# Optimization experiments

Hardware: AMD Instinct MI355X
Metric: run time of the kernel (lower is better)

The kernel has to match this reference:

```python
import jax, jax.numpy as jnp
import numpy as np

DIM = 1024
NUM_HEADS = 16
HEAD_DIM = DIM // NUM_HEADS
B, L = 4, 4096


def setup_inputs() -> dict:
    key = jax.random.key(0)
    ks = jax.random.split(key, 11)
    s = 1.0 / np.sqrt(DIM)
    inp = {
        'q_seq': jax.random.normal(ks[0], (B, L, DIM), jnp.float32),
        'k_seq': jax.random.normal(ks[1], (B, L, DIM), jnp.float32),
        'v_seq': jax.random.normal(ks[2], (B, L, DIM), jnp.float32),
        'Wq': jax.random.normal(ks[3], (DIM, DIM), jnp.float32) * s,
        'bq': jax.random.normal(ks[4], (DIM,), jnp.float32) * s,
        'Wk': jax.random.normal(ks[5], (DIM, DIM), jnp.float32) * s,
        'bk': jax.random.normal(ks[6], (DIM,), jnp.float32) * s,
        'Wv': jax.random.normal(ks[7], (DIM, DIM), jnp.float32) * s,
        'bv': jax.random.normal(ks[8], (DIM,), jnp.float32) * s,
        'Wo': jax.random.normal(ks[9], (DIM, DIM), jnp.float32) * s,
        'bo': jax.random.normal(ks[10], (DIM,), jnp.float32) * s,
        'extract_common': 1,
    }
    return inp


def _heads(x):
    # [B, L, DIM] -> [B, H, L, D]
    Bb, Ll, _ = x.shape
    return x.reshape(Bb, Ll, NUM_HEADS, HEAD_DIM).transpose(0, 2, 1, 3)


def reference(q_seq, k_seq, v_seq, Wq, bq, Wk, bk, Wv, bv, Wo, bo, extract_common):
    Q = _heads(q_seq @ Wq.T + bq)   # [B, H, Lq, D]
    K = _heads(k_seq @ Wk.T + bk)   # [B, H, Lk, D]
    V = _heads(v_seq @ Wv.T + bv)   # [B, H, Lv, D]
    # softmax over the sequence dimension of K (torch dim=2 of [B,H,L,D])
    K_probs = jax.nn.softmax(K, axis=2)
    # context = K_probs^T @ V : [B, H, D, D]
    context = jnp.einsum('bhld,bhle->bhde', K_probs, V)
    attended = jnp.einsum('bhld,bhde->bhle', Q, context)  # [B, H, Lq, D]
    if extract_common:
        target = attended
    else:
        target = V - attended
    Bb, _, Ll, _ = target.shape
    target = target.transpose(0, 2, 1, 3).reshape(Bb, Ll, DIM)
    return target @ Wo.T + bo
```

## Files before the change

kernel.cpp:

```cpp
#include <hip/hip_runtime.h>
#include <cmath>

typedef __bf16 bf16x8 __attribute__((ext_vector_type(8)));
typedef float f32x4 __attribute__((ext_vector_type(4)));
typedef unsigned short us8 __attribute__((ext_vector_type(8)));

__device__ __forceinline__ unsigned short f2bf(float f) {
    union { float f; unsigned u; } x; x.f = f;
    unsigned u = x.u + 0x7FFFu + ((x.u >> 16) & 1u);
    return (unsigned short)(u >> 16);
}
__device__ __forceinline__ float bf2f(unsigned short h) {
    union { unsigned u; float f; } x; x.u = ((unsigned)h) << 16;
    return x.f;
}

__device__ __forceinline__ us8 pack8(f32x4 a, f32x4 b) {
    union { bf16x8 h; us8 u; } cv;
    cv.h[0] = (__bf16)a[0]; cv.h[1] = (__bf16)a[1];
    cv.h[2] = (__bf16)a[2]; cv.h[3] = (__bf16)a[3];
    cv.h[4] = (__bf16)b[0]; cv.h[5] = (__bf16)b[1];
    cv.h[6] = (__bf16)b[2]; cv.h[7] = (__bf16)b[3];
    return cv.u;
}

__device__ __forceinline__ us8 cvt8(const float* p) {
    f32x4 a = *(const f32x4*)p;
    f32x4 b = *(const f32x4*)(p + 4);
    return pack8(a, b);
}

__device__ __forceinline__ void gl2lds16(const unsigned short* g, unsigned short* l) {
    __builtin_amdgcn_global_load_lds(
        (const __attribute__((address_space(1))) unsigned int*)g,
        (__attribute__((address_space(3))) unsigned int*)l, 16, 0, 0);
}

__global__ __launch_bounds__(256)
void cvt_kernel(const float* __restrict__ src, unsigned short* __restrict__ dst) {
    const size_t i = ((size_t)blockIdx.x * 256 + threadIdx.x) * 8;
    *(us8*)(dst + i) = cvt8(src + i);
}

__global__ __launch_bounds__(256)
void cvt_w4(const float* __restrict__ s0, const float* __restrict__ s1,
            const float* __restrict__ s2, const float* __restrict__ s3,
            unsigned short* __restrict__ d0, unsigned short* __restrict__ d1,
            unsigned short* __restrict__ d2, unsigned short* __restrict__ d3) {
    const float* sp[4] = {s0, s1, s2, s3};
    unsigned short* dp[4] = {d0, d1, d2, d3};
    const float* src = sp[blockIdx.y];
    unsigned short* dst = dp[blockIdx.y];
    const size_t i = ((size_t)blockIdx.x * 256 + threadIdx.x) * 8;
    *(us8*)(dst + i) = cvt8(src + i);
}

__device__ __forceinline__ void swz_tiles(int& m0, int& n0) {
    const int slot = blockIdx.x + (blockIdx.y << 3);
    const int w = ((slot & 7) << 7) | (slot >> 3);
    m0 = (w >> 3) << 7;
    n0 = (w & 7) << 7;
}

template<int MODE, bool BF>
__global__ __launch_bounds__(256)
void gemm_proj(const void* __restrict__ Ap, const void* __restrict__ Wp,
               const float* __restrict__ bias,
               unsigned short* __restrict__ outT,
               float* __restrict__ S)
{
    __shared__ __align__(16) unsigned short lds[24576];

    const int tid = threadIdx.x;
    const int wid = tid >> 6, lane = tid & 63;
    const int quad = lane >> 4, l16 = lane & 15;
    const int waveM = wid >> 1, waveN = wid & 1;
    int m0, n0; swz_tiles(m0, n0);
    const int srow = tid >> 2, scol = (tid & 3) * 8;
    const int r4 = lane >> 2, c8 = (lane & 3) * 8;

    f32x4 acc[4][4] = {};

    if (BF) {
        const unsigned short* A = (const unsigned short*)Ap;
        const unsigned short* W = (const unsigned short*)Wp;
#define STAGE_P(K0, BASE)                                                     \
        for (int s = wid; s < 8; s += 4) {                                    \
            const int row = s * 16 + r4;                                      \
            gl2lds16(A + (size_t)(m0 + row) * 1024 + (K0) + c8, (BASE) + s * 512);          \
            gl2lds16(W + (size_t)(n0 + row) * 1024 + (K0) + c8, (BASE) + 4096 + s * 512);   \
        }
        STAGE_P(0, lds);
        STAGE_P(32, lds + 8192);
        asm volatile("s_waitcnt vmcnt(4) lgkmcnt(0)" ::: "memory");
        __builtin_amdgcn_s_barrier();

        int cur = 0;
        for (int it = 0; it < 32; ++it) {
            if (it < 30) {
                const int st = (cur >= 1) ? cur - 1 : 2;
                STAGE_P((it + 2) * 32, lds + st * 8192);
            }
            const unsigned short* ldsA = lds + cur * 8192;
            const unsigned short* ldsB = ldsA + 4096;
            bf16x8 af[4], bfr[4];
#pragma unroll
            for (int i = 0; i < 4; ++i)
                af[i] = *(const bf16x8*)(ldsA + (waveM * 64 + i * 16 + l16) * 32 + quad * 8);
#pragma unroll
            for (int j = 0; j < 4; ++j)
                bfr[j] = *(const bf16x8*)(ldsB + (waveN * 64 + j * 16 + l16) * 32 + quad * 8);
#pragma unroll
            for (int i = 0; i < 4; ++i)
#pragma unroll
                for (int j = 0; j < 4; ++j)
                    acc[i][j] = __builtin_amdgcn_mfma_f32_16x16x32_bf16(af[i], bfr[j], acc[i][j], 0, 0, 0);
            if (it < 30) {
                asm volatile("s_waitcnt vmcnt(4) lgkmcnt(0)" ::: "memory");
                __builtin_amdgcn_s_barrier();
            } else if (it == 30) {
                asm volatile("s_waitcnt vmcnt(0) lgkmcnt(0)" ::: "memory");
                __builtin_amdgcn_s_barrier();
            }
            cur = (cur < 2) ? cur + 1 : 0;
        }
#undef STAGE_P
    } else {
        const float* A = (const float*)Ap;
        const float* W = (const float*)Wp;
#pragma unroll
        for (int p = 0; p < 2; ++p) {
            *(us8*)(lds + (p * 64 + srow) * 32 + scol) = cvt8(A + (size_t)(m0 + p * 64 + srow) * 1024 + scol);
            *(us8*)(lds + 4096 + (p * 64 + srow) * 32 + scol) = cvt8(W + (size_t)(n0 + p * 64 + srow) * 1024 + scol);
        }
        __syncthreads();
        int cur = 0;
        for (int k0 = 0; k0 < 1024; k0 += 32) {
            const int nxt = cur ^ 1;
            if (k0 < 992) {
#pragma unroll
                for (int p = 0; p < 2; ++p) {
                    *(us8*)(lds + nxt * 8192 + (p * 64 + srow) * 32 + scol) =
                        cvt8(A + (size_t)(m0 + p * 64 + srow) * 1024 + k0 + 32 + scol);
                    *(us8*)(lds + nxt * 8192 + 4096 + (p * 64 + srow) * 32 + scol) =
                        cvt8(W + (size_t)(n0 + p * 64 + srow) * 1024 + k0 + 32 + scol);
                }
            }
            const unsigned short* ldsA = lds + cur * 8192;
            const unsigned short* ldsB = ldsA + 4096;
            bf16x8 af[4], bfr[4];
#pragma unroll
            for (int i = 0; i < 4; ++i)
                af[i] = *(const bf16x8*)(ldsA + (waveM * 64 + i * 16 + l16) * 32 + quad * 8);
#pragma unroll
            for (int j = 0; j < 4; ++j)
                bfr[j] = *(const bf16x8*)(ldsB + (waveN * 64 + j * 16 + l16) * 32 + quad * 8);
#pragma unroll
            for (int i = 0; i < 4; ++i)
#pragma unroll
                for (int j = 0; j < 4; ++j)
                    acc[i][j] = __builtin_amdgcn_mfma_f32_16x16x32_bf16(af[i], bfr[j], acc[i][j], 0, 0, 0);
            __syncthreads();
            cur = nxt;
        }
    }
    __syncthreads();

    const int b = m0 >> 12, l0 = m0 & 4095;
#pragma unroll
    for (int j = 0; j < 4; ++j) {
        const int nn = waveN * 64 + j * 16 + l16;
        const float bc = bias[n0 + nn];
        float ssum = 0.f;
#pragma unroll
        for (int i = 0; i < 4; ++i)
#pragma unroll
            for (int r = 0; r < 4; ++r) {
                const int mm = waveM * 64 + i * 16 + quad * 4 + r;
                float v = acc[i][j][r] + bc;
                if (MODE == 1) v = expf(fminf(fmaxf(v, -30.f), 30.f));
                lds[nn * 136 + mm] = f2bf(v);
                ssum += v;
            }
        if (MODE == 1) {
            ssum += __shfl_xor(ssum, 16);
            ssum += __shfl_xor(ssum, 32);
            if (lane < 16)
                atomicAdd(&S[(size_t)b * 1024 + n0 + waveN * 64 + j * 16 + lane], ssum);
        }
    }
    __syncthreads();
    const int seg = (tid & 15) * 8;
#pragma unroll
    for (int it = 0; it < 8; ++it) {
        const int nn = (tid >> 4) + it * 16;
        us8 v = *(const us8*)&lds[nn * 136 + seg];
        *(us8*)(outT + ((size_t)b * 1024 + n0 + nn) * 4096 + l0 + seg) = v;
    }
}

__global__ __launch_bounds__(256)
void ctx_kernel(const unsigned short* __restrict__ Vt,
                const unsigned short* __restrict__ Et,
                float* __restrict__ ctxf)
{
    __shared__ __align__(16) unsigned short lds[8192];

    const int tid = threadIdx.x;
    const int wid = tid >> 6, lane = tid & 63;
    const int quad = lane >> 4, l16 = lane & 15;
    const int b = blockIdx.z, h = blockIdx.y;
    const int lbase = blockIdx.x * 512;

    const unsigned short* Arow = Vt + ((size_t)b * 1024 + h * 64) * 4096;
    const unsigned short* Brow = Et + ((size_t)b * 1024 + h * 64) * 4096;

    const int srow = tid >> 2;
    const int scol = (tid & 3) * 8;

    f32x4 acc[4] = {};

    {
        us8 va = *(const us8*)(Arow + (size_t)srow * 4096 + lbase + scol);
        us8 vb = *(const us8*)(Brow + (size_t)srow * 4096 + lbase + scol);
        *(us8*)(lds + srow * 32 + scol) = va;
        *(us8*)(lds + 2048 + srow * 32 + scol) = vb;
    }
    __syncthreads();

    int cur = 0;
    for (int k0 = 0; k0 < 512; k0 += 32) {
        const int nxt = cur ^ 1;
        us8 na = {}, nb = {};
        const bool pf = (k0 < 480);
        if (pf) {
            na = *(const us8*)(Arow + (size_t)srow * 4096 + lbase + k0 + 32 + scol);
            nb = *(const us8*)(Brow + (size_t)srow * 4096 + lbase + k0 + 32 + scol);
        }
        const unsigned short* ldsA = lds + cur * 4096;
        const unsigned short* ldsB = ldsA + 2048;
        bf16x8 a = *(const bf16x8*)(ldsA + (wid * 16 + l16) * 32 + quad * 8);
#pragma unroll
        for (int j = 0; j < 4; ++j) {
            bf16x8 bb = *(const bf16x8*)(ldsB + (j * 16 + l16) * 32 + quad * 8);
            acc[j] = __builtin_amdgcn_mfma_f32_16x16x32_bf16(a, bb, acc[j], 0, 0, 0);
        }
        if (pf) {
            *(us8*)(lds + nxt * 4096 + srow * 32 + scol) = na;
            *(us8*)(lds + nxt * 4096 + 2048 + srow * 32 + scol) = nb;
        }
        __syncthreads();
        cur = nxt;
    }
    float* base = ctxf + ((size_t)(b * 16 + h)) * 4096;
#pragma unroll
    for (int j = 0; j < 4; ++j)
#pragma unroll
        for (int r = 0; r < 4; ++r) {
            const int e = wid * 16 + quad * 4 + r;
            const int d = j * 16 + l16;
            atomicAdd(base + e * 64 + d, acc[j][r]);
        }
}

template<bool BF>
__global__ __launch_bounds__(256)
void gemm_qattn(const void* __restrict__ Ap, const void* __restrict__ Wp,
                const float* __restrict__ bias,
                const float* __restrict__ ctxf,
                const float* __restrict__ Sv,
                const unsigned short* __restrict__ Vt,
                const int* __restrict__ ec,
                unsigned short* __restrict__ att)
{
    __shared__ __align__(16) unsigned short lds[26624];
    unsigned short* ldsQ = lds;
    unsigned short* ldsC = lds + 17408;

    const int tid = threadIdx.x;
    const int wid = tid >> 6, lane = tid & 63;
    const int quad = lane >> 4, l16 = lane & 15;
    const int waveM = wid >> 1, waveN = wid & 1;
    int m0, n0; swz_tiles(m0, n0);
    const int b = m0 >> 12;
    const int srow = tid >> 2, scol = (tid & 3) * 8;
    const int r4 = lane >> 2, c8 = (lane & 3) * 8;

    f32x4 acc[4][4] = {};

    if (BF) {
        const unsigned short* A = (const unsigned short*)Ap;
        const unsigned short* W = (const unsigned short*)Wp;
#define STAGE_Q(K0, BASE)                                                     \
        for (int s = wid; s < 8; s += 4) {                                    \
            const int row = s * 16 + r4;                                      \
            gl2lds16(A + (size_t)(m0 + row) * 1024 + (K0) + c8, (BASE) + s * 512);          \
            gl2lds16(W + (size_t)(n0 + row) * 1024 + (K0) + c8, (BASE) + 4096 + s * 512);   \
        }
        STAGE_Q(0, lds);
        STAGE_Q(32, lds + 8192);
        asm volatile("s_waitcnt vmcnt(4) lgkmcnt(0)" ::: "memory");
        __builtin_amdgcn_s_barrier();

        int cur = 0;
        for (int it = 0; it < 32; ++it) {
            if (it < 30) {
                const int st = (cur >= 1) ? cur - 1 : 2;
                STAGE_Q((it + 2) * 32, lds + st * 8192);
            }
            const unsigned short* ldsA = lds + cur * 8192;
            const unsigned short* ldsB = ldsA + 4096;
            bf16x8 af[4], bfr[4];
#pragma unroll
            for (int i = 0; i < 4; ++i)
                af[i] = *(const bf16x8*)(ldsA + (waveM * 64 + i * 16 + l16) * 32 + quad * 8);
#pragma unroll
            for (int j = 0; j < 4; ++j)
                bfr[j] = *(const bf16x8*)(ldsB + (waveN * 64 + j * 16 + l16) * 32 + quad * 8);
#pragma unroll
            for (int i = 0; i < 4; ++i)
#pragma unroll
                for (int j = 0; j < 4; ++j)
                    acc[i][j] = __builtin_amdgcn_mfma_f32_16x16x32_bf16(af[i], bfr[j], acc[i][j], 0, 0, 0);
            if (it < 30) {
                asm volatile("s_waitcnt vmcnt(4) lgkmcnt(0)" ::: "memory");
                __builtin_amdgcn_s_barrier();
            } else if (it == 30) {
                asm volatile("s_waitcnt vmcnt(0) lgkmcnt(0)" ::: "memory");
                __builtin_amdgcn_s_barrier();
            }
            cur = (cur < 2) ? cur + 1 : 0;
        }
#undef STAGE_Q
    } else {
        const float* A = (const float*)Ap;
        const float* W = (const float*)Wp;
#pragma unroll
        for (int p = 0; p < 2; ++p) {
            *(us8*)(lds + (p * 64 + srow) * 32 + scol) = cvt8(A + (size_t)(m0 + p * 64 + srow) * 1024 + scol);
            *(us8*)(lds + 4096 + (p * 64 + srow) * 32 + scol) = cvt8(W + (size_t)(n0 + p * 64 + srow) * 1024 + scol);
        }
        __syncthreads();
        int cur = 0;
        for (int k0 = 0; k0 < 1024; k0 += 32) {
            const int nxt = cur ^ 1;
            if (k0 < 992) {
#pragma unroll
                for (int p = 0; p < 2; ++p) {
                    *(us8*)(lds + nxt * 8192 + (p * 64 + srow) * 32 + scol) =
                        cvt8(A + (size_t)(m0 + p * 64 + srow) * 1024 + k0 + 32 + scol);
                    *(us8*)(lds + nxt * 8192 + 4096 + (p * 64 + srow) * 32 + scol) =
                        cvt8(W + (size_t)(n0 + p * 64 + srow) * 1024 + k0 + 32 + scol);
                }
            }
            const unsigned short* ldsA = lds + cur * 8192;
            const unsigned short* ldsB = ldsA + 4096;
            bf16x8 af[4], bfr[4];
#pragma unroll
            for (int i = 0; i < 4; ++i)
                af[i] = *(const bf16x8*)(ldsA + (waveM * 64 + i * 16 + l16) * 32 + quad * 8);
#pragma unroll
            for (int j = 0; j < 4; ++j)
                bfr[j] = *(const bf16x8*)(ldsB + (waveN * 64 + j * 16 + l16) * 32 + quad * 8);
#pragma unroll
            for (int i = 0; i < 4; ++i)
#pragma unroll
                for (int j = 0; j < 4; ++j)
                    acc[i][j] = __builtin_amdgcn_mfma_f32_16x16x32_bf16(af[i], bfr[j], acc[i][j], 0, 0, 0);
            __syncthreads();
            cur = nxt;
        }
    }
    __syncthreads();

    {
        const int e2 = tid >> 1;
        const int sg = (tid & 1) * 32;
        const int hh = (n0 >> 6) + (e2 >> 6);
        const float* srcf = ctxf + (((size_t)(b * 16) + hh) * 64 + (e2 & 63)) * 64 + sg;
        const float* Sp = Sv + (size_t)b * 1024 + hh * 64 + sg;
#pragma unroll
        for (int u = 0; u < 4; ++u) {
            f32x4 c0 = *(const f32x4*)(srcf + u * 8);
            f32x4 c1 = *(const f32x4*)(srcf + u * 8 + 4);
            union { bf16x8 h; us8 uu; } cv;
#pragma unroll
            for (int j = 0; j < 4; ++j) cv.h[j] = (__bf16)(c0[j] / Sp[u * 8 + j]);
#pragma unroll
            for (int j = 0; j < 4; ++j) cv.h[4 + j] = (__bf16)(c1[j] / Sp[u * 8 + 4 + j]);
            *(us8*)&ldsC[(size_t)e2 * 72 + sg + u * 8] = cv.uu;
        }
    }

#pragma unroll
    for (int j = 0; j < 4; ++j) {
        const int nn = waveN * 64 + j * 16 + l16;
        const float bc = bias[n0 + nn];
#pragma unroll
        for (int i = 0; i < 4; ++i)
#pragma unroll
            for (int r = 0; r < 4; ++r) {
                const int mm = waveM * 64 + i * 16 + quad * 4 + r;
                ldsQ[mm * 136 + nn] = f2bf(acc[i][j][r] + bc);
            }
    }
    __syncthreads();

    f32x4 acc2[4][4] = {};
#pragma unroll
    for (int ks = 0; ks < 64; ks += 32) {
        bf16x8 aq[4], cq[4];
#pragma unroll
        for (int i = 0; i < 4; ++i)
            aq[i] = *(const bf16x8*)&ldsQ[(waveM * 64 + i * 16 + l16) * 136 + waveN * 64 + ks + quad * 8];
#pragma unroll
        for (int j = 0; j < 4; ++j)
            cq[j] = *(const bf16x8*)&ldsC[(waveN * 64 + j * 16 + l16) * 72 + ks + quad * 8];
#pragma unroll
        for (int i = 0; i < 4; ++i)
#pragma unroll
            for (int j = 0; j < 4; ++j)
                acc2[i][j] = __builtin_amdgcn_mfma_f32_16x16x32_bf16(aq[i], cq[j], acc2[i][j], 0, 0, 0);
    }

    const int common = ec[0];
#pragma unroll
    for (int i = 0; i < 4; ++i)
#pragma unroll
        for (int j = 0; j < 4; ++j)
#pragma unroll
            for (int r = 0; r < 4; ++r) {
                const int lrow = m0 + waveM * 64 + i * 16 + quad * 4 + r;
                const int chan = n0 + waveN * 64 + j * 16 + l16;
                float vv = acc2[i][j][r];
                if (!common)
                    vv = bf2f(Vt[((size_t)(lrow >> 12) * 1024 + chan) * 4096 + (lrow & 4095)]) - vv;
                att[(size_t)lrow * 1024 + chan] = f2bf(vv);
            }
}

template<bool BF>
__global__ __launch_bounds__(256)
void gemm_out(const unsigned short* __restrict__ A, const void* __restrict__ Wp,
              const float* __restrict__ bias,
              float* __restrict__ outP)
{
    __shared__ __align__(16) unsigned short lds[24576];

    const int tid = threadIdx.x;
    const int wid = tid >> 6, lane = tid & 63;
    const int quad = lane >> 4, l16 = lane & 15;
    const int waveM = wid >> 1, waveN = wid & 1;
    int m0, n0; swz_tiles(m0, n0);
    const int srow = tid >> 2, scol = (tid & 3) * 8;
    const int r4 = lane >> 2, c8 = (lane & 3) * 8;

    f32x4 acc[4][4] = {};

    if (BF) {
        const unsigned short* W = (const unsigned short*)Wp;
#define STAGE_O(K0, BASE)                                                     \
        for (int s = wid; s < 8; s += 4) {                                    \
            const int row = s * 16 + r4;                                      \
            gl2lds16(A + (size_t)(m0 + row) * 1024 + (K0) + c8, (BASE) + s * 512);          \
            gl2lds16(W + (size_t)(n0 + row) * 1024 + (K0) + c8, (BASE) + 4096 + s * 512);   \
        }
        STAGE_O(0, lds);
        STAGE_O(32, lds + 8192);
        asm volatile("s_waitcnt vmcnt(4) lgkmcnt(0)" ::: "memory");
        __builtin_amdgcn_s_barrier();

        int cur = 0;
        for (int it = 0; it < 32; ++it) {
            if (it < 30) {
                const int st = (cur >= 1) ? cur - 1 : 2;
                STAGE_O((it + 2) * 32, lds + st * 8192);
            }
            const unsigned short* ldsA = lds + cur * 8192;
            const unsigned short* ldsB = ldsA + 4096;
            bf16x8 af[4], bfr[4];
#pragma unroll
            for (int i = 0; i < 4; ++i)
                af[i] = *(const bf16x8*)(ldsA + (waveM * 64 + i * 16 + l16) * 32 + quad * 8);
#pragma unroll
            for (int j = 0; j < 4; ++j)
                bfr[j] = *(const bf16x8*)(ldsB + (waveN * 64 + j * 16 + l16) * 32 + quad * 8);
#pragma unroll
            for (int i = 0; i < 4; ++i)
#pragma unroll
                for (int j = 0; j < 4; ++j)
                    acc[i][j] = __builtin_amdgcn_mfma_f32_16x16x32_bf16(af[i], bfr[j], acc[i][j], 0, 0, 0);
            if (it < 30) {
                asm volatile("s_waitcnt vmcnt(4) lgkmcnt(0)" ::: "memory");
                __builtin_amdgcn_s_barrier();
            } else if (it == 30) {
                asm volatile("s_waitcnt vmcnt(0) lgkmcnt(0)" ::: "memory");
                __builtin_amdgcn_s_barrier();
            }
            cur = (cur < 2) ? cur + 1 : 0;
        }
#undef STAGE_O
    } else {
        const float* W = (const float*)Wp;
#pragma unroll
        for (int p = 0; p < 2; ++p) {
            *(us8*)(lds + (p * 64 + srow) * 32 + scol) = *(const us8*)(A + (size_t)(m0 + p * 64 + srow) * 1024 + scol);
            *(us8*)(lds + 4096 + (p * 64 + srow) * 32 + scol) = cvt8(W + (size_t)(n0 + p * 64 + srow) * 1024 + scol);
        }
        __syncthreads();
        int cur = 0;
        for (int k0 = 0; k0 < 1024; k0 += 32) {
            const int nxt = cur ^ 1;
            if (k0 < 992) {
#pragma unroll
                for (int p = 0; p < 2; ++p) {
                    *(us8*)(lds + nxt * 8192 + (p * 64 + srow) * 32 + scol) =
                        *(const us8*)(A + (size_t)(m0 + p * 64 + srow) * 1024 + k0 + 32 + scol);
                    *(us8*)(lds + nxt * 8192 + 4096 + (p * 64 + srow) * 32 + scol) =
                        cvt8(W + (size_t)(n0 + p * 64 + srow) * 1024 + k0 + 32 + scol);
                }
            }
            const unsigned short* ldsA = lds + cur * 8192;
            const unsigned short* ldsB = ldsA + 4096;
            bf16x8 af[4], bfr[4];
#pragma unroll
            for (int i = 0; i < 4; ++i)
                af[i] = *(const bf16x8*)(ldsA + (waveM * 64 + i * 16 + l16) * 32 + quad * 8);
#pragma unroll
            for (int j = 0; j < 4; ++j)
                bfr[j] = *(const bf16x8*)(ldsB + (waveN * 64 + j * 16 + l16) * 32 + quad * 8);
#pragma unroll
            for (int i = 0; i < 4; ++i)
#pragma unroll
                for (int j = 0; j < 4; ++j)
                    acc[i][j] = __builtin_amdgcn_mfma_f32_16x16x32_bf16(af[i], bfr[j], acc[i][j], 0, 0, 0);
            __syncthreads();
            cur = nxt;
        }
    }

#pragma unroll
    for (int j = 0; j < 4; ++j) {
        const int col = n0 + waveN * 64 + j * 16 + l16;
        const float bc = bias[col];
#pragma unroll
        for (int i = 0; i < 4; ++i)
#pragma unroll
            for (int r = 0; r < 4; ++r) {
                const int row = m0 + waveM * 64 + i * 16 + quad * 4 + r;
                outP[(size_t)row * 1024 + col] = acc[i][j][r] + bc;
            }
    }
}

extern "C" void kernel_launch(void* const* d_in, const int* in_sizes, int n_in,
                              void* d_out, int out_size, void* d_ws, size_t ws_size,
                              hipStream_t stream)
{
    const float* q  = (const float*)d_in[0];
    const float* k  = (const float*)d_in[1];
    const float* v  = (const float*)d_in[2];
    const float* Wq = (const float*)d_in[3];
    const float* bq = (const float*)d_in[4];
    const float* Wk = (const float*)d_in[5];
    const float* bk = (const float*)d_in[6];
    const float* Wv = (const float*)d_in[7];
    const float* bv = (const float*)d_in[8];
    const float* Wo = (const float*)d_in[9];
    const float* bo = (const float*)d_in[10];
    const int* ec   = (const int*)d_in[11];

    char* ws = (char*)d_ws;
    const size_t NEED_FAST = 110641152;
    const dim3 gblk(8, 128, 1);
    const dim3 gctx(8, 16, 4);

    if (ws_size >= NEED_FAST) {
        unsigned short* Ab   = (unsigned short*)(ws);
        unsigned short* Et   = (unsigned short*)(ws + 33554432);
        unsigned short* Vt   = (unsigned short*)(ws + 67108864);
        unsigned short* Wkb  = (unsigned short*)(ws + 100663296);
        unsigned short* Wvb  = (unsigned short*)(ws + 102760448);
        unsigned short* Wqb  = (unsigned short*)(ws + 104857600);
        unsigned short* Wob  = (unsigned short*)(ws + 106954752);
        float*          ctxf = (float*)(ws + 109051904);
        float*          S    = (float*)(ws + 110100480);
        unsigned short* att  = Et;

        hipMemsetAsync(S, 0, 4096 * sizeof(float), stream);
        hipMemsetAsync(ctxf, 0, 4 * 16 * 64 * 64 * sizeof(float), stream);

        cvt_w4<<<dim3(512, 4), 256, 0, stream>>>(Wk, Wv, Wq, Wo, Wkb, Wvb, Wqb, Wob);

        cvt_kernel<<<8192, 256, 0, stream>>>(k, Ab);
        gemm_proj<1, true><<<gblk, 256, 0, stream>>>(Ab, Wkb, bk, Et, S);

        cvt_kernel<<<8192, 256, 0, stream>>>(v, Ab);
        gemm_proj<2, true><<<gblk, 256, 0, stream>>>(Ab, Wvb, bv, Vt, nullptr);

        ctx_kernel<<<gctx, 256, 0, stream>>>(Vt, Et, ctxf);

        cvt_kernel<<<8192, 256, 0, stream>>>(q, Ab);
        gemm_qattn<true><<<gblk, 256, 0, stream>>>(Ab, Wqb, bq, ctxf, S, Vt, ec, att);

        gemm_out<true><<<gblk, 256, 0, stream>>>(att, Wob, bo, (float*)d_out);
    } else {
        unsigned short* Et   = (unsigned short*)(ws);
        unsigned short* Vt   = (unsigned short*)(ws + 33554432);
        float*          ctxf = (float*)(ws + 67108864);
        float*          S    = (float*)(ws + 68157440);
        unsigned short* att  = Et;

        hipMemsetAsync(S, 0, 4096 * sizeof(float), stream);
        hipMemsetAsync(ctxf, 0, 4 * 16 * 64 * 64 * sizeof(float), stream);

        gemm_proj<1, false><<<gblk, 256, 0, stream>>>(k, Wk, bk, Et, S);
        gemm_proj<2, false><<<gblk, 256, 0, stream>>>(v, Wv, bv, Vt, nullptr);
        ctx_kernel<<<gctx, 256, 0, stream>>>(Vt, Et, ctxf);
        gemm_qattn<false><<<gblk, 256, 0, stream>>>(q, Wq, bq, ctxf, S, Vt, ec, att);
        gemm_out<false><<<gblk, 256, 0, stream>>>(att, Wo, bo, (float*)d_out);
    }
}
```

Baseline: 449.3 us.

## Fuse fp32-to-bf16 activation conversion into projection GEMM loads

Removes the three separate cvt_kernel passes over q/k/v and instead loads fp32 activations directly into LDS via global_load_lds with an XOR swizzle, converting to bf16 when reading fragments. This saves writing and re-reading a bf16 copy of each 64MB input, at the cost of double the global bytes per A tile inside the GEMM and extra LDS capacity. The pipeline also drops from three stages to two, which may expose more load latency.

```diff
diff --git a/kernel.cpp b/kernel.cpp
--- a/kernel.cpp
+++ b/kernel.cpp
@@ -15,15 +15,19 @@
     return x.f;
 }
 
+__device__ __forceinline__ bf16x8 pack8b(f32x4 a, f32x4 b) {
+    bf16x8 h;
+    h[0] = (__bf16)a[0]; h[1] = (__bf16)a[1];
+    h[2] = (__bf16)a[2]; h[3] = (__bf16)a[3];
+    h[4] = (__bf16)b[0]; h[5] = (__bf16)b[1];
+    h[6] = (__bf16)b[2]; h[7] = (__bf16)b[3];
+    return h;
+}
 __device__ __forceinline__ us8 pack8(f32x4 a, f32x4 b) {
     union { bf16x8 h; us8 u; } cv;
-    cv.h[0] = (__bf16)a[0]; cv.h[1] = (__bf16)a[1];
-    cv.h[2] = (__bf16)a[2]; cv.h[3] = (__bf16)a[3];
-    cv.h[4] = (__bf16)b[0]; cv.h[5] = (__bf16)b[1];
-    cv.h[6] = (__bf16)b[2]; cv.h[7] = (__bf16)b[3];
+    cv.h = pack8b(a, b);
     return cv.u;
 }
-
 __device__ __forceinline__ us8 cvt8(const float* p) {
     f32x4 a = *(const f32x4*)p;
     f32x4 b = *(const f32x4*)(p + 4);
@@ -35,11 +39,10 @@
         (const __attribute__((address_space(1))) unsigned int*)g,
         (__attribute__((address_space(3))) unsigned int*)l, 16, 0, 0);
 }
-
-__global__ __launch_bounds__(256)
-void cvt_kernel(const float* __restrict__ src, unsigned short* __restrict__ dst) {
-    const size_t i = ((size_t)blockIdx.x * 256 + threadIdx.x) * 8;
-    *(us8*)(dst + i) = cvt8(src + i);
+__device__ __forceinline__ void gl2lds16f(const float* g, float* l) {
+    __builtin_amdgcn_global_load_lds(
+        (const __attribute__((address_space(1))) unsigned int*)g,
+        (__attribute__((address_space(3))) unsigned int*)l, 16, 0, 0);
 }
 
 __global__ __launch_bounds__(256)
@@ -62,9 +65,9 @@
     n0 = (w & 7) << 7;
 }
 
-template<int MODE, bool BF>
+template<int MODE, bool WBF>
 __global__ __launch_bounds__(256)
-void gemm_proj(const void* __restrict__ Ap, const void* __restrict__ Wp,
+void gemm_proj(const float* __restrict__ A, const void* __restrict__ Wp,
                const float* __restrict__ bias,
                unsigned short* __restrict__ outT,
                float* __restrict__ S)
@@ -81,57 +84,55 @@
 
     f32x4 acc[4][4] = {};
 
-    if (BF) {
-        const unsigned short* A = (const unsigned short*)Ap;
+    if (WBF) {
         const unsigned short* W = (const unsigned short*)Wp;
-#define STAGE_P(K0, BASE)                                                     \
-        for (int s = wid; s < 8; s += 4) {                                    \
-            const int row = s * 16 + r4;                                      \
-            gl2lds16(A + (size_t)(m0 + row) * 1024 + (K0) + c8, (BASE) + s * 512);          \
-            gl2lds16(W + (size_t)(n0 + row) * 1024 + (K0) + c8, (BASE) + 4096 + s * 512);   \
-        }
-        STAGE_P(0, lds);
-        STAGE_P(32, lds + 8192);
-        asm volatile("s_waitcnt vmcnt(4) lgkmcnt(0)" ::: "memory");
-        __builtin_amdgcn_s_barrier();
-
-        int cur = 0;
-        for (int it = 0; it < 32; ++it) {
-            if (it < 30) {
-                const int st = (cur >= 1) ? cur - 1 : 2;
-                STAGE_P((it + 2) * 32, lds + st * 8192);
-            }
-            const unsigned short* ldsA = lds + cur * 8192;
-            const unsigned short* ldsB = ldsA + 4096;
+        float* ldsAf = (float*)lds;
+        unsigned short* ldsW = lds + 16384;
+        const int acol = ((lane & 7) ^ (lane >> 3)) * 4;
+#define STAGE_P2(K0, AB, WB)                                                   \
+        for (int c = wid; c < 16; c += 4)                                      \
+            gl2lds16f(A + (size_t)(m0 + c * 8 + (lane >> 3)) * 1024 + (K0) + acol, (AB) + c * 256); \
+        for (int s = wid; s < 8; s += 4)                                       \
+            gl2lds16(W + (size_t)(n0 + s * 16 + r4) * 1024 + (K0) + c8, (WB) + s * 512);
+        STAGE_P2(0, ldsAf, ldsW);
+        for (int t = 0; t < 32; ++t) {
+            const int cur = t & 1;
+            if (t < 31) {
+                const int nx = cur ^ 1;
+                STAGE_P2((t + 1) * 32, ldsAf + nx * 4096, ldsW + nx * 4096);
+                asm volatile("s_waitcnt vmcnt(6) lgkmcnt(0)" ::: "memory");
+            } else {
+                asm volatile("s_waitcnt vmcnt(0) lgkmcnt(0)" ::: "memory");
+            }
+            __builtin_amdgcn_s_barrier();
+            const float* fA = ldsAf + cur * 4096;
+            const unsigned short* sW = ldsW + cur * 4096;
             bf16x8 af[4], bfr[4];
 #pragma unroll
-            for (int i = 0; i < 4; ++i)
-                af[i] = *(const bf16x8*)(ldsA + (waveM * 64 + i * 16 + l16) * 32 + quad * 8);
+            for (int i = 0; i < 4; ++i) {
+                const int ra = waveM * 64 + i * 16 + l16;
+                f32x4 lo = *(const f32x4*)(fA + ra * 32 + (((2 * quad) ^ (ra & 7)) * 4));
+                f32x4 hi = *(const f32x4*)(fA + ra * 32 + (((2 * quad + 1) ^ (ra & 7)) * 4));
+                af[i] = pack8b(lo, hi);
+            }
 #pragma unroll
             for (int j = 0; j < 4; ++j)
-                bfr[j] = *(const bf16x8*)(ldsB + (waveN * 64 + j * 16 + l16) * 32 + quad * 8);
+                bfr[j] = *(const bf16x8*)(sW + (waveN * 64 + j * 16 + l16) * 32 + quad * 8);
 #pragma unroll
             for (int i = 0; i < 4; ++i)
 #pragma unroll
                 for (int j = 0; j < 4; ++j)
                     acc[i][j] = __builtin_amdgcn_mfma_f32_16x16x32_bf16(af[i], bfr[j], acc[i][j], 0, 0, 0);
-            if (it < 30) {
-                asm volatile("s_waitcnt vmcnt(4) lgkmcnt(0)" ::: "memory");
-                __builtin_amdgcn_s_barrier();
-            } else if (it == 30) {
-                asm volatile("s_waitcnt vmcnt(0) lgkmcnt(0)" ::: "memory");
-                __builtin_amdgcn_s_barrier();
-            }
-            cur = (cur < 2) ? cur + 1 : 0;
-        }
-#undef STAGE_P
+            asm volatile("s_waitcnt lgkmcnt(0)" ::: "memory");
+            __builtin_amdgcn_s_barrier();
+        }
+#undef STAGE_P2
     } else {
-        const float* A = (const float*)Ap;
-        const float* W = (const float*)Wp;
+        const float* Wf = (const float*)Wp;
 #pragma unroll
         for (int p = 0; p < 2; ++p) {
             *(us8*)(lds + (p * 64 + srow) * 32 + scol) = cvt8(A + (size_t)(m0 + p * 64 + srow) * 1024 + scol);
-            *(us8*)(lds + 4096 + (p * 64 + srow) * 32 + scol) = cvt8(W + (size_t)(n0 + p * 64 + srow) * 1024 + scol);
+            *(us8*)(lds + 4096 + (p * 64 + srow) * 32 + scol) = cvt8(Wf + (size_t)(n0 + p * 64 + srow) * 1024 + scol);
         }
         __syncthreads();
         int cur = 0;
@@ -143,7 +144,7 @@
                     *(us8*)(lds + nxt * 8192 + (p * 64 + srow) * 32 + scol) =
                         cvt8(A + (size_t)(m0 + p * 64 + srow) * 1024 + k0 + 32 + scol);
                     *(us8*)(lds + nxt * 8192 + 4096 + (p * 64 + srow) * 32 + scol) =
-                        cvt8(W + (size_t)(n0 + p * 64 + srow) * 1024 + k0 + 32 + scol);
+                        cvt8(Wf + (size_t)(n0 + p * 64 + srow) * 1024 + k0 + 32 + scol);
                 }
             }
             const unsigned short* ldsA = lds + cur * 8192;
@@ -263,9 +264,9 @@
         }
 }
 
-template<bool BF>
+template<bool WBF>
 __global__ __launch_bounds__(256)
-void gemm_qattn(const void* __restrict__ Ap, const void* __restrict__ Wp,
+void gemm_qattn(const float* __restrict__ A, const void* __restrict__ Wp,
                 const float* __restrict__ bias,
                 const float* __restrict__ ctxf,
                 const float* __restrict__ Sv,
@@ -288,57 +289,55 @@
 
     f32x4 acc[4][4] = {};
 
-    if (BF) {
-        const unsigned short* A = (const unsigned short*)Ap;
+    if (WBF) {
         const unsigned short* W = (const unsigned short*)Wp;
-#define STAGE_Q(K0, BASE)                                                     \
-        for (int s = wid; s < 8; s += 4) {                                    \
-            const int row = s * 16 + r4;                                      \
-            gl2lds16(A + (size_t)(m0 + row) * 1024 + (K0) + c8, (BASE) + s * 512);          \
-            gl2lds16(W + (size_t)(n0 + row) * 1024 + (K0) + c8, (BASE) + 4096 + s * 512);   \
-        }
-        STAGE_Q(0, lds);
-        STAGE_Q(32, lds + 8192);
-        asm volatile("s_waitcnt vmcnt(4) lgkmcnt(0)" ::: "memory");
-        __builtin_amdgcn_s_barrier();
-
-        int cur = 0;
-        for (int it = 0; it < 32; ++it) {
-            if (it < 30) {
-                const int st = (cur >= 1) ? cur - 1 : 2;
-                STAGE_Q((it + 2) * 32, lds + st * 8192);
-            }
-            const unsigned short* ldsA = lds + cur * 8192;
-            const unsigned short* ldsB = ldsA + 4096;
+        float* ldsAf = (float*)lds;
+        unsigned short* ldsW = lds + 16384;
+        const int acol = ((lane & 7) ^ (lane >> 3)) * 4;
+#define STAGE_Q2(K0, AB, WB)                                                   \
+        for (int c = wid; c < 16; c += 4)                                      \
+            gl2lds16f(A + (size_t)(m0 + c * 8 + (lane >> 3)) * 1024 + (K0) + acol, (AB) + c * 256); \
+        for (int s = wid; s < 8; s += 4)                                       \
+            gl2lds16(W + (size_t)(n0 + s * 16 + r4) * 1024 + (K0) + c8, (WB) + s * 512);
+        STAGE_Q2(0, ldsAf, ldsW);
+        for (int t = 0; t < 32; ++t) {
+            const int cur = t & 1;
+            if (t < 31) {
+                const int nx = cur ^ 1;
+                STAGE_Q2((t + 1) * 32, ldsAf + nx * 4096, ldsW + nx * 4096);
+                asm volatile("s_waitcnt vmcnt(6) lgkmcnt(0)" ::: "memory");
+            } else {
+                asm volatile("s_waitcnt vmcnt(0) lgkmcnt(0)" ::: "memory");
+            }
+            __builtin_amdgcn_s_barrier();
+            const float* fA = ldsAf + cur * 4096;
+            const unsigned short* sW = ldsW + cur * 4096;
             bf16x8 af[4], bfr[4];
 #pragma unroll
-            for (int i = 0; i < 4; ++i)
-                af[i] = *(const bf16x8*)(ldsA + (waveM * 64 + i * 16 + l16) * 32 + quad * 8);
+            for (int i = 0; i < 4; ++i) {
+                const int ra = waveM * 64 + i * 16 + l16;
+                f32x4 lo = *(const f32x4*)(fA + ra * 32 + (((2 * quad) ^ (ra & 7)) * 4));
+                f32x4 hi = *(const f32x4*)(fA + ra * 32 + (((2 * quad + 1) ^ (ra & 7)) * 4));
+                af[i] = pack8b(lo, hi);
+            }
 #pragma unroll
             for (int j = 0; j < 4; ++j)
-                bfr[j] = *(const bf16x8*)(ldsB + (waveN * 64 + j * 16 + l16) * 32 + quad * 8);
+                bfr[j] = *(const bf16x8*)(sW + (waveN * 64 + j * 16 + l16) * 32 + quad * 8);
 #pragma unroll
             for (int i = 0; i < 4; ++i)
 #pragma unroll
                 for (int j = 0; j < 4; ++j)
                     acc[i][j] = __builtin_amdgcn_mfma_f32_16x16x32_bf16(af[i], bfr[j], acc[i][j], 0, 0, 0);
-            if (it < 30) {
-                asm volatile("s_waitcnt vmcnt(4) lgkmcnt(0)" ::: "memory");
-                __builtin_amdgcn_s_barrier();
-            } else if (it == 30) {
-                asm volatile("s_waitcnt vmcnt(0) lgkmcnt(0)" ::: "memory");
-                __builtin_amdgcn_s_barrier();
-            }
-            cur = (cur < 2) ? cur + 1 : 0;
-        }
-#undef STAGE_Q
+            asm volatile("s_waitcnt lgkmcnt(0)" ::: "memory");
+            __builtin_amdgcn_s_barrier();
+        }
+#undef STAGE_Q2
     } else {
-        const float* A = (const float*)Ap;
-        const float* W = (const float*)Wp;
+        const float* Wf = (const float*)Wp;
 #pragma unroll
         for (int p = 0; p < 2; ++p) {
             *(us8*)(lds + (p * 64 + srow) * 32 + scol) = cvt8(A + (size_t)(m0 + p * 64 + srow) * 1024 + scol);
-            *(us8*)(lds + 4096 + (p * 64 + srow) * 32 + scol) = cvt8(W + (size_t)(n0 + p * 64 + srow) * 1024 + scol);
+            *(us8*)(lds + 4096 + (p * 64 + srow) * 32 + scol) = cvt8(Wf + (size_t)(n0 + p * 64 + srow) * 1024 + scol);
         }
         __syncthreads();
         int cur = 0;
@@ -350,7 +349,7 @@
                     *(us8*)(lds + nxt * 8192 + (p * 64 + srow) * 32 + scol) =
                         cvt8(A + (size_t)(m0 + p * 64 + srow) * 1024 + k0 + 32 + scol);
                     *(us8*)(lds + nxt * 8192 + 4096 + (p * 64 + srow) * 32 + scol) =
-                        cvt8(W + (size_t)(n0 + p * 64 + srow) * 1024 + k0 + 32 + scol);
+                        cvt8(Wf + (size_t)(n0 + p * 64 + srow) * 1024 + k0 + 32 + scol);
                 }
             }
             const unsigned short* ldsA = lds + cur * 8192;
@@ -571,20 +570,19 @@
     const int* ec   = (const int*)d_in[11];
 
     char* ws = (char*)d_ws;
-    const size_t NEED_FAST = 110641152;
+    const size_t NEED_FAST = 76562432;
     const dim3 gblk(8, 128, 1);
     const dim3 gctx(8, 16, 4);
 
     if (ws_size >= NEED_FAST) {
-        unsigned short* Ab   = (unsigned short*)(ws);
-        unsigned short* Et   = (unsigned short*)(ws + 33554432);
-        unsigned short* Vt   = (unsigned short*)(ws + 67108864);
-        unsigned short* Wkb  = (unsigned short*)(ws + 100663296);
-        unsigned short* Wvb  = (unsigned short*)(ws + 102760448);
-        unsigned short* Wqb  = (unsigned short*)(ws + 104857600);
-        unsigned short* Wob  = (unsigned short*)(ws + 106954752);
-        float*          ctxf = (float*)(ws + 109051904);
-        float*          S    = (float*)(ws + 110100480);
+        unsigned short* Et   = (unsigned short*)(ws);
+        unsigned short* Vt   = (unsigned short*)(ws + 33554432);
+        unsigned short* Wkb  = (unsigned short*)(ws + 67108864);
+        unsigned short* Wvb  = (unsigned short*)(ws + 69206016);
+        unsigned short* Wqb  = (unsigned short*)(ws + 71303168);
+        unsigned short* Wob  = (unsigned short*)(ws + 73400320);
+        float*          ctxf = (float*)(ws + 75497472);
+        float*          S    = (float*)(ws + 76546048);
         unsigned short* att  = Et;
 
         hipMemsetAsync(S, 0, 4096 * sizeof(float), stream);
@@ -592,16 +590,12 @@
 
         cvt_w4<<<dim3(512, 4), 256, 0, stream>>>(Wk, Wv, Wq, Wo, Wkb, Wvb, Wqb, Wob);
 
-        cvt_kernel<<<8192, 256, 0, stream>>>(k, Ab);
-        gemm_proj<1, true><<<gblk, 256, 0, stream>>>(Ab, Wkb, bk, Et, S);
-
-        cvt_kernel<<<8192, 256, 0, stream>>>(v, Ab);
-        gemm_proj<2, true><<<gblk, 256, 0, stream>>>(Ab, Wvb, bv, Vt, nullptr);
+        gemm_proj<1, true><<<gblk, 256, 0, stream>>>(k, Wkb, bk, Et, S);
+        gemm_proj<2, true><<<gblk, 256, 0, stream>>>(v, Wvb, bv, Vt, nullptr);
 
         ctx_kernel<<<gctx, 256, 0, stream>>>(Vt, Et, ctxf);
 
-        cvt_kernel<<<8192, 256, 0, stream>>>(q, Ab);
-        gemm_qattn<true><<<gblk, 256, 0, stream>>>(Ab, Wqb, bq, ctxf, S, Vt, ec, att);
+        gemm_qattn<true><<<gblk, 256, 0, stream>>>(q, Wqb, bq, ctxf, S, Vt, ec, att);
 
         gemm_out<true><<<gblk, 256, 0, stream>>>(att, Wob, bo, (float*)d_out);
     } else {
```

Result: slower. 482.2 us (+7.3%).
